# Optimization experiments

Measured on AMD Instinct MI355X. Metric: run time of the kernel, lower is better.

## Reference

```python
import jax, jax.numpy as jnp
import numpy as np

EPS = 1e-12  # F.normalize eps

def _layer(x, adj, y, mask, w, b):
    # support = x @ W
    support = x @ w
    a = adj * mask
    # row-wise L1 normalize: a / max(sum|a|, eps)
    norm = jnp.maximum(jnp.sum(jnp.abs(a), axis=1, keepdims=True), EPS)
    a = a / norm
    out = a @ support + b
    y_hat = a @ y
    return out, y_hat

def setup_inputs() -> dict:
    key = jax.random.key(0)
    ks = jax.random.split(key, 9)
    N, F, H, C = 8192, 512, 256, 40
    stdv1 = 1.0 / np.sqrt(H)
    stdv2 = 1.0 / np.sqrt(C)
    return {
        "x": jax.random.normal(ks[0], (N, F), jnp.float32),
        "adj": jax.random.uniform(ks[1], (N, N), jnp.float32),
        "y": jax.random.uniform(ks[2], (N, C), jnp.float32),
        "mask1": jax.random.uniform(ks[3], (N, N), jnp.float32),
        "mask2": jax.random.uniform(ks[4], (N, N), jnp.float32),
        "w1": jax.random.uniform(ks[5], (F, H), jnp.float32, -stdv1, stdv1),
        "b1": jax.random.uniform(ks[6], (H,), jnp.float32, -stdv1, stdv1),
        "w2": jax.random.uniform(ks[7], (H, C), jnp.float32, -stdv2, stdv2),
        "b2": jax.random.uniform(ks[8], (C,), jnp.float32, -stdv2, stdv2),
    }

def reference(x, adj, y, mask1, mask2, w1, b1, w2, b2):
    h, y_hat = _layer(x, adj, y, mask1, w1, b1)
    h = jax.nn.relu(h)  # dropout is identity in eval mode
    h, y_hat = _layer(h, adj, y_hat, mask2, w2, b2)
    return jax.nn.log_softmax(h, axis=1), jax.nn.log_softmax(y_hat, axis=1)
```

## Files before the change

kernel.cpp:

```cpp
#include <hip/hip_runtime.h>
#include <cstdint>
#include <cstddef>

typedef float f32x4 __attribute__((ext_vector_type(4)));
typedef __bf16 bf16x8_t __attribute__((ext_vector_type(8)));
typedef short s16x8_t __attribute__((ext_vector_type(8)));
typedef unsigned short u16x4_t __attribute__((ext_vector_type(4)));

#define NN 8192
#define FD 512
#define HD 256
#define CD 40

static __device__ __forceinline__ unsigned short f2bf(float f) {
    unsigned int u = __builtin_bit_cast(unsigned int, f);
    u += 0x7FFFu + ((u >> 16) & 1u);
    return (unsigned short)(u >> 16);
}
static __device__ __forceinline__ float bf2f(unsigned short s) {
    unsigned int u = ((unsigned int)s) << 16;
    return __builtin_bit_cast(float, u);
}

typedef __attribute__((address_space(3))) unsigned int lds_u32_t;
typedef __attribute__((address_space(1))) const unsigned int gbl_u32_t;
static __device__ __forceinline__ void gload16(const void* g, const void* lds) {
    __builtin_amdgcn_global_load_lds((gbl_u32_t*)g, (lds_u32_t*)lds, 16, 0, 0);
}

__global__ __launch_bounds__(256) void k_prep_xw1(
        const float* __restrict__ adj,
        const float* __restrict__ mask1,
        const float* __restrict__ mask2,
        unsigned short* __restrict__ P1,
        unsigned short* __restrict__ P2,
        float* __restrict__ sinv1,
        float* __restrict__ sinv2,
        const float* __restrict__ x,
        const float* __restrict__ w1,
        float* __restrict__ sup1) {
    __shared__ float xs[64][36];
    __shared__ float ws[32][68];
    __shared__ float red1[4], red2[4];
    const int t = threadIdx.x;

    if (blockIdx.x < 512) {
        const int bid = blockIdx.x;
        const int m0 = (bid >> 2) * 64;
        const int n0 = (bid & 3) * 64;
        const int tx = t & 15, ty = t >> 4;
        float acc[4][4] = {};
        for (int k0 = 0; k0 < FD; k0 += 32) {
            for (int i = t; i < 512; i += 256) {
                int r = i >> 3, c = (i & 7) << 2;
                *(float4*)&xs[r][c] = *(const float4*)&x[(size_t)(m0 + r) * FD + k0 + c];
            }
            for (int i = t; i < 512; i += 256) {
                int r = i >> 4, c = (i & 15) << 2;
                *(float4*)&ws[r][c] = *(const float4*)&w1[(size_t)(k0 + r) * HD + n0 + c];
            }
            __syncthreads();
            for (int k = 0; k < 32; ++k) {
                float a_[4], b_[4];
                #pragma unroll
                for (int i = 0; i < 4; ++i) a_[i] = xs[ty * 4 + i][k];
                #pragma unroll
                for (int j = 0; j < 4; ++j) b_[j] = ws[k][tx * 4 + j];
                #pragma unroll
                for (int i = 0; i < 4; ++i)
                    #pragma unroll
                    for (int j = 0; j < 4; ++j) acc[i][j] += a_[i] * b_[j];
            }
            __syncthreads();
        }
        #pragma unroll
        for (int i = 0; i < 4; ++i)
            #pragma unroll
            for (int j = 0; j < 4; ++j)
                sup1[(size_t)(m0 + ty * 4 + i) * HD + n0 + tx * 4 + j] = acc[i][j];
        return;
    }

    const int row = blockIdx.x - 512;
    const f32x4* __restrict__ ar  = (const f32x4*)(adj   + (size_t)row * NN);
    const f32x4* __restrict__ m1r = (const f32x4*)(mask1 + (size_t)row * NN);
    const f32x4* __restrict__ m2r = mask2 ? (const f32x4*)(mask2 + (size_t)row * NN) : nullptr;
    float s1 = 0.f, s2 = 0.f;

    f32x4 a  = __builtin_nontemporal_load(&ar[t]);
    f32x4 m1 = __builtin_nontemporal_load(&m1r[t]);
    f32x4 m2 = {};
    if (m2r) m2 = __builtin_nontemporal_load(&m2r[t]);

    #pragma unroll
    for (int j = 0; j < 8; ++j) {
        const int idx = j * 256 + t;
        f32x4 an = {}, m1n = {}, m2n = {};
        if (j < 7) {
            an  = __builtin_nontemporal_load(&ar[idx + 256]);
            m1n = __builtin_nontemporal_load(&m1r[idx + 256]);
            if (m2r) m2n = __builtin_nontemporal_load(&m2r[idx + 256]);
        }
        {
            const float p0 = a[0] * m1[0], p1 = a[1] * m1[1], p2 = a[2] * m1[2], p3 = a[3] * m1[3];
            s1 += fabsf(p0) + fabsf(p1) + fabsf(p2) + fabsf(p3);
            u16x4_t pk; pk.x = f2bf(p0); pk.y = f2bf(p1); pk.z = f2bf(p2); pk.w = f2bf(p3);
            *(u16x4_t*)&P1[(size_t)row * NN + idx * 4] = pk;
        }
        if (m2r) {
            const float p0 = a[0] * m2[0], p1 = a[1] * m2[1], p2 = a[2] * m2[2], p3 = a[3] * m2[3];
            s2 += fabsf(p0) + fabsf(p1) + fabsf(p2) + fabsf(p3);
            u16x4_t pk; pk.x = f2bf(p0); pk.y = f2bf(p1); pk.z = f2bf(p2); pk.w = f2bf(p3);
            *(u16x4_t*)&P2[(size_t)row * NN + idx * 4] = pk;
        }
        a = an; m1 = m1n; m2 = m2n;
    }
    #pragma unroll
    for (int d = 32; d; d >>= 1) { s1 += __shfl_xor(s1, d, 64); s2 += __shfl_xor(s2, d, 64); }
    if ((t & 63) == 0) { red1[t >> 6] = s1; red2[t >> 6] = s2; }
    __syncthreads();
    if (t == 0) {
        const float a1 = red1[0] + red1[1] + red1[2] + red1[3];
        sinv1[row] = 1.0f / fmaxf(a1, 1e-12f);
        if (sinv2) {
            const float a2 = red2[0] + red2[1] + red2[2] + red2[3];
            sinv2[row] = 1.0f / fmaxf(a2, 1e-12f);
        }
    }
}

__global__ __launch_bounds__(256) void k_prep(const float* __restrict__ adj,
                                              const float* __restrict__ mask1,
                                              const float* __restrict__ mask2,
                                              unsigned short* __restrict__ P1,
                                              unsigned short* __restrict__ P2,
                                              float* __restrict__ sinv1,
                                              float* __restrict__ sinv2) {
    const int row = blockIdx.x;
    const int t = threadIdx.x;
    const f32x4* __restrict__ ar  = (const f32x4*)(adj   + (size_t)row * NN);
    const f32x4* __restrict__ m1r = (const f32x4*)(mask1 + (size_t)row * NN);
    const f32x4* __restrict__ m2r = mask2 ? (const f32x4*)(mask2 + (size_t)row * NN) : nullptr;
    float s1 = 0.f, s2 = 0.f;

    f32x4 a  = __builtin_nontemporal_load(&ar[t]);
    f32x4 m1 = __builtin_nontemporal_load(&m1r[t]);
    f32x4 m2 = {};
    if (m2r) m2 = __builtin_nontemporal_load(&m2r[t]);

    #pragma unroll
    for (int j = 0; j < 8; ++j) {
        const int idx = j * 256 + t;
        f32x4 an = {}, m1n = {}, m2n = {};
        if (j < 7) {
            an  = __builtin_nontemporal_load(&ar[idx + 256]);
            m1n = __builtin_nontemporal_load(&m1r[idx + 256]);
            if (m2r) m2n = __builtin_nontemporal_load(&m2r[idx + 256]);
        }
        {
            const float p0 = a[0] * m1[0], p1 = a[1] * m1[1], p2 = a[2] * m1[2], p3 = a[3] * m1[3];
            s1 += fabsf(p0) + fabsf(p1) + fabsf(p2) + fabsf(p3);
            u16x4_t pk; pk.x = f2bf(p0); pk.y = f2bf(p1); pk.z = f2bf(p2); pk.w = f2bf(p3);
            *(u16x4_t*)&P1[(size_t)row * NN + idx * 4] = pk;
        }
        if (m2r) {
            const float p0 = a[0] * m2[0], p1 = a[1] * m2[1], p2 = a[2] * m2[2], p3 = a[3] * m2[3];
            s2 += fabsf(p0) + fabsf(p1) + fabsf(p2) + fabsf(p3);
            u16x4_t pk; pk.x = f2bf(p0); pk.y = f2bf(p1); pk.z = f2bf(p2); pk.w = f2bf(p3);
            *(u16x4_t*)&P2[(size_t)row * NN + idx * 4] = pk;
        }
        a = an; m1 = m1n; m2 = m2n;
    }
    __shared__ float red1[4], red2[4];
    #pragma unroll
    for (int d = 32; d; d >>= 1) { s1 += __shfl_xor(s1, d, 64); s2 += __shfl_xor(s2, d, 64); }
    if ((t & 63) == 0) { red1[t >> 6] = s1; red2[t >> 6] = s2; }
    __syncthreads();
    if (t == 0) {
        const float a1 = red1[0] + red1[1] + red1[2] + red1[3];
        sinv1[row] = 1.0f / fmaxf(a1, 1e-12f);
        if (sinv2) {
            const float a2 = red2[0] + red2[1] + red2[2] + red2[3];
            sinv2[row] = 1.0f / fmaxf(a2, 1e-12f);
        }
    }
}

__global__ __launch_bounds__(256) void k_packB1T(const float* __restrict__ sup1,
                                                 const float* __restrict__ y,
                                                 unsigned short* __restrict__ B1T) {
    __shared__ float tl[64][33];
    const int kt = blockIdx.x & 127;
    const int nt = blockIdx.x >> 7;
    const int k0 = kt * 64, n0 = nt * 32;
    const int t = threadIdx.x;
    {
        const int kr = t >> 2, cb = (t & 3) * 8;
        #pragma unroll
        for (int j = 0; j < 8; ++j) {
            const int n = n0 + cb + j;
            float v;
            if (n < 256)      v = sup1[(size_t)(k0 + kr) * HD + n];
            else if (n < 296) v = y[(size_t)(k0 + kr) * CD + (n - 256)];
            else              v = 0.f;
            tl[kr][cb + j] = v;
        }
    }
    __syncthreads();
    {
        const int nr = t >> 3, part = t & 7;
        unsigned short tmp[8];
        #pragma unroll
        for (int j = 0; j < 8; ++j) tmp[j] = f2bf(tl[part * 8 + j][nr]);
        *(s16x8_t*)&B1T[(size_t)(n0 + nr) * NN + k0 + part * 8] = *(s16x8_t*)tmp;
    }
}

template<int BN, int WM, int WN, int SPLIT, int NTILES>
__global__ __launch_bounds__(256) void k_gemm(const unsigned short* __restrict__ A,
                                              const unsigned short* __restrict__ Bt,
                                              float* __restrict__ Cp) {
    constexpr int BM = 128, BK = 64;
    constexpr int MF = BM / (WM * 16);
    constexpr int NF = BN / (WN * 16);
    constexpr int NBI = BN / 32;
    constexpr int NSTR = NTILES * BN;
    constexpr int MT = NN / BM;
    __shared__ unsigned short As[BM * BK];
    __shared__ unsigned short Bs[BN * BK];
    int mt, ks, nt;
    if constexpr (NTILES > 1) {
        constexpr int NXCD = 8;
        constexpr int PAIRS = MT * SPLIT;
        static_assert(PAIRS % NXCD == 0, "pair count must split across XCDs");
        constexpr int PPX = PAIRS / NXCD;
        const int L = blockIdx.x;
        const int x = L % NXCD, q = L / NXCD;
        const int pr = x * PPX + q / NTILES;
        nt = q % NTILES;
        mt = pr / SPLIT;
        ks = pr % SPLIT;
    } else {
        int b = blockIdx.x;
        nt = 0;
        ks = b % SPLIT;  b /= SPLIT;
        mt = b;
    }
    const int m0 = mt * BM, n0 = nt * BN;
    const int t = threadIdx.x, w = t >> 6, ln = t & 63;
    const int wn = w % WN, wm = w / WN;
    const int lrow = ln & 15, lkq = ln >> 4;
    const int kbeg = ks * (NN / SPLIT), kend = kbeg + (NN / SPLIT);

    f32x4 acc[MF][NF] = {};
    for (int kb = kbeg; kb < kend; kb += BK) {
        #pragma unroll
        for (int i = 0; i < 4; ++i) {
            const int off = (w * 4 + i) * 1024 + ln * 16;
            const int r = off >> 7, ch = (off >> 4) & 7;
            gload16(A + (size_t)(m0 + r) * NN + kb + ((ch ^ (r & 7)) << 3),
                    &As[(w * 4 + i) * 512]);
        }
        #pragma unroll
        for (int i = 0; i < NBI; ++i) {
            const int off = (w * NBI + i) * 1024 + ln * 16;
            const int r = off >> 7, ch = (off >> 4) & 7;
            gload16(Bt + (size_t)(n0 + r) * NN + kb + ((ch ^ (r & 7)) << 3),
                    &Bs[(w * NBI + i) * 512]);
        }
        __syncthreads();

        bf16x8_t af[MF][2];
        #pragma unroll
        for (int mf = 0; mf < MF; ++mf)
            #pragma unroll
            for (int kh = 0; kh < 2; ++kh) {
                const int r = wm * (MF * 16) + mf * 16 + lrow;
                const int ch = (kh * 4 + lkq) ^ (r & 7);
                af[mf][kh] = __builtin_bit_cast(bf16x8_t, *(const s16x8_t*)&As[r * 64 + ch * 8]);
            }
        bf16x8_t bfr[NF][2];
        #pragma unroll
        for (int nf = 0; nf < NF; ++nf)
            #pragma unroll
            for (int kh = 0; kh < 2; ++kh) {
                const int r = wn * (NF * 16) + nf * 16 + lrow;
                const int ch = (kh * 4 + lkq) ^ (r & 7);
                bfr[nf][kh] = __builtin_bit_cast(bf16x8_t, *(const s16x8_t*)&Bs[r * 64 + ch * 8]);
            }
        #pragma unroll
        for (int kh = 0; kh < 2; ++kh)
            #pragma unroll
            for (int mf = 0; mf < MF; ++mf)
                #pragma unroll
                for (int nf = 0; nf < NF; ++nf)
                    acc[mf][nf] = __builtin_amdgcn_mfma_f32_16x16x32_bf16(
                        af[mf][kh], bfr[nf][kh], acc[mf][nf], 0, 0, 0);
        __syncthreads();
    }
    #pragma unroll
    for (int mf = 0; mf < MF; ++mf)
        #pragma unroll
        for (int nf = 0; nf < NF; ++nf)
            #pragma unroll
            for (int e = 0; e < 4; ++e) {
                const int m = m0 + wm * (MF * 16) + mf * 16 + lkq * 4 + e;
                const int n = n0 + wn * (NF * 16) + nf * 16 + lrow;
                Cp[((size_t)ks * NN + m) * NSTR + n] = acc[mf][nf][e];
            }
}

__global__ __launch_bounds__(256) void k_finC(const float* __restrict__ U,
                                              const float* __restrict__ sinv1,
                                              const float* __restrict__ b1,
                                              unsigned short* __restrict__ h1,
                                              unsigned short* __restrict__ B2T) {
    const int t = threadIdx.x;
    const int r = t >> 3, l8 = t & 7;
    const int m = blockIdx.x * 32 + r;
    const float si = sinv1[m];
    const float* __restrict__ u0 = U + (size_t)m * 320;
    const float* __restrict__ u1 = U + (size_t)(NN + m) * 320;
    #pragma unroll
    for (int i = 0; i < 10; ++i) {
        const int c = (l8 + i * 8) * 4;
        f32x4 a = *(const f32x4*)&u0[c];
        f32x4 b = *(const f32x4*)&u1[c];
        f32x4 v;
        #pragma unroll
        for (int e = 0; e < 4; ++e) v[e] = (a[e] + b[e]) * si;
        if (i < 8) {
            u16x4_t pk;
            #pragma unroll
            for (int e = 0; e < 4; ++e) {
                const float hv = fmaxf(v[e] + b1[c + e], 0.f);
                ((unsigned short*)&pk)[e] = f2bf(hv);
            }
            *(u16x4_t*)&h1[(size_t)m * HD + c] = pk;
        } else {
            #pragma unroll
            for (int e = 0; e < 4; ++e) {
                const int cc = c + e;
                if (cc < 296) B2T[(size_t)(40 + cc - 256) * NN + m] = f2bf(v[e]);
            }
        }
    }
}

__global__ __launch_bounds__(256) void k_hw2(const unsigned short* __restrict__ h1,
                                             const float* __restrict__ w2,
                                             unsigned short* __restrict__ B2T) {
    __shared__ float w2s[HD * CD];
    __shared__ unsigned short h1s[32][264];
    __shared__ float ot[CD][33];
    const int t = threadIdx.x;
    const int mb = blockIdx.x * 32;
    for (int i = t; i < HD * CD; i += 256) w2s[i] = w2[i];
    for (int i = t; i < 1024; i += 256) {
        const int r = i >> 5, c = (i & 31) * 8;
        *(s16x8_t*)&h1s[r][c] = *(const s16x8_t*)&h1[(size_t)(mb + r) * HD + c];
    }
    __syncthreads();
    const int m = t >> 3, n0 = t & 7;
    float a5[5] = {};
    for (int k = 0; k < HD; ++k) {
        const float hv = bf2f(h1s[m][k]);
        #pragma unroll
        for (int j = 0; j < 5; ++j) a5[j] += hv * w2s[k * CD + n0 + 8 * j];
    }
    #pragma unroll
    for (int j = 0; j < 5; ++j) ot[n0 + 8 * j][m] = a5[j];
    __syncthreads();
    for (int i = t; i < CD * 32; i += 256) {
        const int n = i >> 5, mm = i & 31;
        B2T[(size_t)n * NN + mb + mm] = f2bf(ot[n][mm]);
    }
    for (int i = t; i < 16 * 32; i += 256)
        B2T[(size_t)(80 + (i >> 5)) * NN + mb + (i & 31)] = 0;
}

__global__ __launch_bounds__(256) void k_finD(const float* __restrict__ U,
                                              const float* __restrict__ sinv2,
                                              const float* __restrict__ b2,
                                              float* __restrict__ out) {
    __shared__ float vt[32][100];
    const int t = threadIdx.x;
    const int mb = blockIdx.x * 32;
    for (int i = t; i < 32 * 24; i += 256) {
        const int r = i / 24, f4 = i % 24;
        const int m = mb + r;
        f32x4 s = {};
        #pragma unroll
        for (int p = 0; p < 8; ++p) {
            f32x4 v = *(const f32x4*)&U[((size_t)p * NN + m) * 96 + f4 * 4];
            #pragma unroll
            for (int e = 0; e < 4; ++e) s[e] += v[e];
        }
        const float si = sinv2[m];
        #pragma unroll
        for (int e = 0; e < 4; ++e) {
            const int c = f4 * 4 + e;
            float v = s[e] * si;
            if (c < CD) v += b2[c];
            vt[r][c] = v;
        }
    }
    __syncthreads();
    const int l8 = t & 7;
    #pragma unroll
    for (int pass = 0; pass < 2; ++pass) {
        const int task = pass * 32 + (t >> 3);
        const int row = task & 31, mat = task >> 5;
        float vals[5];
        float mx = -3.0e38f;
        #pragma unroll
        for (int j = 0; j < 5; ++j) { vals[j] = vt[row][mat * CD + l8 + 8 * j]; mx = fmaxf(mx, vals[j]); }
        mx = fmaxf(mx, __shfl_xor(mx, 4, 8));
        mx = fmaxf(mx, __shfl_xor(mx, 2, 8));
        mx = fmaxf(mx, __shfl_xor(mx, 1, 8));
        float se = 0.f;
        #pragma unroll
        for (int j = 0; j < 5; ++j) se += expf(vals[j] - mx);
        se += __shfl_xor(se, 4, 8);
        se += __shfl_xor(se, 2, 8);
        se += __shfl_xor(se, 1, 8);
        const float ls = logf(se);
        float* op = out + (size_t)mat * (NN * CD) + (size_t)(mb + row) * CD;
        #pragma unroll
        for (int j = 0; j < 5; ++j) op[l8 + 8 * j] = vals[j] - mx - ls;
    }
}

extern "C" void kernel_launch(void* const* d_in, const int* in_sizes, int n_in,
                              void* d_out, int out_size, void* d_ws, size_t ws_size,
                              hipStream_t stream) {
    (void)in_sizes; (void)n_in; (void)out_size;
    const float* x     = (const float*)d_in[0];
    const float* adj   = (const float*)d_in[1];
    const float* y     = (const float*)d_in[2];
    const float* mask1 = (const float*)d_in[3];
    const float* mask2 = (const float*)d_in[4];
    const float* w1    = (const float*)d_in[5];
    const float* b1    = (const float*)d_in[6];
    const float* w2    = (const float*)d_in[7];
    const float* b2    = (const float*)d_in[8];
    float* out = (float*)d_out;

    const bool both = ws_size >= 313065472ULL;
    char* p = (char*)d_ws;
    unsigned short* P1 = (unsigned short*)p; p += 134217728;
    unsigned short* P2 = P1;
    if (both) { P2 = (unsigned short*)p; p += 134217728; }
    float*          sup1 = (float*)p;          p += 8388608;
    unsigned short* B1T  = (unsigned short*)p; p += 5242880;
    unsigned short* h1   = (unsigned short*)p; p += 4194304;
    unsigned short* B2T  = (unsigned short*)p; p += 1572864;
    float*          U    = (float*)p;          p += 25165824;
    float*          sinv1 = (float*)p;         p += 32768;
    float*          sinv2 = (float*)p;         p += 32768;

    if (both) {
        hipLaunchKernelGGL(k_prep_xw1, dim3(8704), dim3(256), 0, stream,
                           adj, mask1, mask2, P1, P2, sinv1, sinv2, x, w1, sup1);
    } else {
        hipLaunchKernelGGL(k_prep_xw1, dim3(8704), dim3(256), 0, stream,
                           adj, mask1, (const float*)nullptr, P1, (unsigned short*)nullptr,
                           sinv1, (float*)nullptr, x, w1, sup1);
    }
    hipLaunchKernelGGL(k_packB1T, dim3(1280), dim3(256), 0, stream, sup1, y, B1T);
    hipLaunchKernelGGL(HIP_KERNEL_NAME(k_gemm<64, 2, 2, 2, 5>), dim3(640), dim3(256), 0, stream,
                       P1, B1T, U);
    hipLaunchKernelGGL(k_finC,    dim3(256),  dim3(256), 0, stream, U, sinv1, b1, h1, B2T);
    hipLaunchKernelGGL(k_hw2,     dim3(256),  dim3(256), 0, stream, h1, w2, B2T);
    if (!both) {
        hipLaunchKernelGGL(k_prep, dim3(8192), dim3(256), 0, stream,
                           adj, mask2, (const float*)nullptr, P1, (unsigned short*)nullptr,
                           sinv2, (float*)nullptr);
    }
    hipLaunchKernelGGL(HIP_KERNEL_NAME(k_gemm<96, 4, 1, 8, 1>), dim3(512), dim3(256), 0, stream,
                       P2, B2T, U);
    hipLaunchKernelGGL(k_finD,    dim3(256),  dim3(256), 0, stream, U, sinv2, b2, out);
}
```

Baseline: 357.3 us.

## Fuse B1T packing into prep kernel and merge finC with hw2

The x@W1 tiles in the prep kernel now transpose through shared memory and write bf16 directly into B1T. Extra blocks in the same launch pack y into B1T and zero its padding rows, so the sup1 buffer and the separate pack kernel go away. finC and hw2 are merged so h1 stays in shared memory instead of round-tripping through global memory. This removes two launches and several intermediate global writes and reads, at the cost of more shared-memory reuse and a larger heterogeneous grid.

```diff
diff --git a/kernel.cpp b/kernel.cpp
--- a/kernel.cpp
+++ b/kernel.cpp
@@ -38,13 +38,14 @@
         float* __restrict__ sinv2,
         const float* __restrict__ x,
         const float* __restrict__ w1,
-        float* __restrict__ sup1) {
-    __shared__ float xs[64][36];
-    __shared__ float ws[32][68];
-    __shared__ float red1[4], red2[4];
+        const float* __restrict__ y,
+        unsigned short* __restrict__ B1T) {
+    __shared__ char smem[18432];
     const int t = threadIdx.x;
 
     if (blockIdx.x < 512) {
+        float (*xs)[36] = (float(*)[36])smem;
+        float (*ws)[68] = (float(*)[68])(smem + 9216);
         const int bid = blockIdx.x;
         const int m0 = (bid >> 2) * 64;
         const int n0 = (bid & 3) * 64;
@@ -73,15 +74,51 @@
             }
             __syncthreads();
         }
+        float (*ot)[65] = (float(*)[65])smem;
         #pragma unroll
         for (int i = 0; i < 4; ++i)
             #pragma unroll
             for (int j = 0; j < 4; ++j)
-                sup1[(size_t)(m0 + ty * 4 + i) * HD + n0 + tx * 4 + j] = acc[i][j];
+                ot[tx * 4 + j][ty * 4 + i] = acc[i][j];
+        __syncthreads();
+        #pragma unroll
+        for (int u = 0; u < 2; ++u) {
+            const int task = t + u * 256;
+            const int nr = task >> 3, part = task & 7;
+            unsigned short tmp[8];
+            #pragma unroll
+            for (int j = 0; j < 8; ++j) tmp[j] = f2bf(ot[nr][part * 8 + j]);
+            *(s16x8_t*)&B1T[(size_t)(n0 + nr) * NN + m0 + part * 8] = *(s16x8_t*)tmp;
+        }
         return;
     }
 
-    const int row = blockIdx.x - 512;
+    if (blockIdx.x < 640) {
+        float (*tl)[41] = (float(*)[41])smem;
+        const int k0 = (blockIdx.x - 512) * 64;
+        for (int u = 0; u < 10; ++u) {
+            const int idx = t + u * 256;
+            tl[idx / 40][idx % 40] = y[(size_t)k0 * CD + idx];
+        }
+        __syncthreads();
+        for (int task = t; task < 320; task += 256) {
+            const int c = task >> 3, part = task & 7;
+            unsigned short tmp[8];
+            #pragma unroll
+            for (int j = 0; j < 8; ++j) tmp[j] = f2bf(tl[part * 8 + j][c]);
+            *(s16x8_t*)&B1T[(size_t)(256 + c) * NN + k0 + part * 8] = *(s16x8_t*)tmp;
+        }
+        for (int task = t; task < 192; task += 256) {
+            const int row = 296 + (task >> 3), part = task & 7;
+            s16x8_t z = {};
+            *(s16x8_t*)&B1T[(size_t)row * NN + k0 + part * 8] = z;
+        }
+        return;
+    }
+
+    float* red1 = (float*)smem;
+    float* red2 = (float*)(smem + 16);
+    const int row = blockIdx.x - 640;
     const f32x4* __restrict__ ar  = (const f32x4*)(adj   + (size_t)row * NN);
     const f32x4* __restrict__ m1r = (const f32x4*)(mask1 + (size_t)row * NN);
     const f32x4* __restrict__ m2r = mask2 ? (const f32x4*)(mask2 + (size_t)row * NN) : nullptr;
@@ -183,36 +220,6 @@
             const float a2 = red2[0] + red2[1] + red2[2] + red2[3];
             sinv2[row] = 1.0f / fmaxf(a2, 1e-12f);
         }
-    }
-}
-
-__global__ __launch_bounds__(256) void k_packB1T(const float* __restrict__ sup1,
-                                                 const float* __restrict__ y,
-                                                 unsigned short* __restrict__ B1T) {
-    __shared__ float tl[64][33];
-    const int kt = blockIdx.x & 127;
-    const int nt = blockIdx.x >> 7;
-    const int k0 = kt * 64, n0 = nt * 32;
-    const int t = threadIdx.x;
-    {
-        const int kr = t >> 2, cb = (t & 3) * 8;
-        #pragma unroll
-        for (int j = 0; j < 8; ++j) {
-            const int n = n0 + cb + j;
-            float v;
-            if (n < 256)      v = sup1[(size_t)(k0 + kr) * HD + n];
-            else if (n < 296) v = y[(size_t)(k0 + kr) * CD + (n - 256)];
-            else              v = 0.f;
-            tl[kr][cb + j] = v;
-        }
-    }
-    __syncthreads();
-    {
-        const int nr = t >> 3, part = t & 7;
-        unsigned short tmp[8];
-        #pragma unroll
-        for (int j = 0; j < 8; ++j) tmp[j] = f2bf(tl[part * 8 + j][nr]);
-        *(s16x8_t*)&B1T[(size_t)(n0 + nr) * NN + k0 + part * 8] = *(s16x8_t*)tmp;
     }
 }
 
@@ -310,70 +317,67 @@
             }
 }
 
-__global__ __launch_bounds__(256) void k_finC(const float* __restrict__ U,
-                                              const float* __restrict__ sinv1,
-                                              const float* __restrict__ b1,
-                                              unsigned short* __restrict__ h1,
-                                              unsigned short* __restrict__ B2T) {
-    const int t = threadIdx.x;
-    const int r = t >> 3, l8 = t & 7;
-    const int m = blockIdx.x * 32 + r;
-    const float si = sinv1[m];
-    const float* __restrict__ u0 = U + (size_t)m * 320;
-    const float* __restrict__ u1 = U + (size_t)(NN + m) * 320;
-    #pragma unroll
-    for (int i = 0; i < 10; ++i) {
-        const int c = (l8 + i * 8) * 4;
-        f32x4 a = *(const f32x4*)&u0[c];
-        f32x4 b = *(const f32x4*)&u1[c];
-        f32x4 v;
-        #pragma unroll
-        for (int e = 0; e < 4; ++e) v[e] = (a[e] + b[e]) * si;
-        if (i < 8) {
-            u16x4_t pk;
-            #pragma unroll
-            for (int e = 0; e < 4; ++e) {
-                const float hv = fmaxf(v[e] + b1[c + e], 0.f);
-                ((unsigned short*)&pk)[e] = f2bf(hv);
-            }
-            *(u16x4_t*)&h1[(size_t)m * HD + c] = pk;
-        } else {
-            #pragma unroll
-            for (int e = 0; e < 4; ++e) {
-                const int cc = c + e;
-                if (cc < 296) B2T[(size_t)(40 + cc - 256) * NN + m] = f2bf(v[e]);
-            }
-        }
-    }
-}
-
-__global__ __launch_bounds__(256) void k_hw2(const unsigned short* __restrict__ h1,
-                                             const float* __restrict__ w2,
-                                             unsigned short* __restrict__ B2T) {
+__global__ __launch_bounds__(256) void k_finC2(const float* __restrict__ U,
+                                               const float* __restrict__ sinv1,
+                                               const float* __restrict__ b1,
+                                               const float* __restrict__ w2,
+                                               unsigned short* __restrict__ B2T) {
     __shared__ float w2s[HD * CD];
     __shared__ unsigned short h1s[32][264];
-    __shared__ float ot[CD][33];
+    __shared__ float otp[CD][33];
     const int t = threadIdx.x;
     const int mb = blockIdx.x * 32;
+
     for (int i = t; i < HD * CD; i += 256) w2s[i] = w2[i];
-    for (int i = t; i < 1024; i += 256) {
-        const int r = i >> 5, c = (i & 31) * 8;
-        *(s16x8_t*)&h1s[r][c] = *(const s16x8_t*)&h1[(size_t)(mb + r) * HD + c];
+
+    {
+        const int r = t >> 3, l8 = t & 7;
+        const int m = mb + r;
+        const float si = sinv1[m];
+        const float* __restrict__ u0 = U + (size_t)m * 320;
+        const float* __restrict__ u1 = U + (size_t)(NN + m) * 320;
+        #pragma unroll
+        for (int i = 0; i < 10; ++i) {
+            const int c = (l8 + i * 8) * 4;
+            f32x4 a = *(const f32x4*)&u0[c];
+            f32x4 b = *(const f32x4*)&u1[c];
+            f32x4 v;
+            #pragma unroll
+            for (int e = 0; e < 4; ++e) v[e] = (a[e] + b[e]) * si;
+            if (i < 8) {
+                u16x4_t pk;
+                #pragma unroll
+                for (int e = 0; e < 4; ++e) {
+                    const float hv = fmaxf(v[e] + b1[c + e], 0.f);
+                    ((unsigned short*)&pk)[e] = f2bf(hv);
+                }
+                *(u16x4_t*)&h1s[r][c] = pk;
+            } else {
+                #pragma unroll
+                for (int e = 0; e < 4; ++e) {
+                    const int cc = c + e;
+                    if (cc < 296) B2T[(size_t)(40 + cc - 256) * NN + m] = f2bf(v[e]);
+                }
+            }
+        }
     }
     __syncthreads();
-    const int m = t >> 3, n0 = t & 7;
-    float a5[5] = {};
-    for (int k = 0; k < HD; ++k) {
-        const float hv = bf2f(h1s[m][k]);
-        #pragma unroll
-        for (int j = 0; j < 5; ++j) a5[j] += hv * w2s[k * CD + n0 + 8 * j];
-    }
-    #pragma unroll
-    for (int j = 0; j < 5; ++j) ot[n0 + 8 * j][m] = a5[j];
+
+    {
+        const int m = t >> 3, n0 = t & 7;
+        float a5[5] = {};
+        for (int k = 0; k < HD; ++k) {
+            const float hv = bf2f(h1s[m][k]);
+            #pragma unroll
+            for (int j = 0; j < 5; ++j) a5[j] += hv * w2s[k * CD + n0 + 8 * j];
+        }
+        #pragma unroll
+        for (int j = 0; j < 5; ++j) otp[n0 + 8 * j][m] = a5[j];
+    }
     __syncthreads();
     for (int i = t; i < CD * 32; i += 256) {
         const int n = i >> 5, mm = i & 31;
-        B2T[(size_t)n * NN + mb + mm] = f2bf(ot[n][mm]);
+        B2T[(size_t)n * NN + mb + mm] = f2bf(otp[n][mm]);
     }
     for (int i = t; i < 16 * 32; i += 256)
         B2T[(size_t)(80 + (i >> 5)) * NN + mb + (i & 31)] = 0;
@@ -451,27 +455,23 @@
     unsigned short* P1 = (unsigned short*)p; p += 134217728;
     unsigned short* P2 = P1;
     if (both) { P2 = (unsigned short*)p; p += 134217728; }
-    float*          sup1 = (float*)p;          p += 8388608;
     unsigned short* B1T  = (unsigned short*)p; p += 5242880;
-    unsigned short* h1   = (unsigned short*)p; p += 4194304;
     unsigned short* B2T  = (unsigned short*)p; p += 1572864;
     float*          U    = (float*)p;          p += 25165824;
     float*          sinv1 = (float*)p;         p += 32768;
     float*          sinv2 = (float*)p;         p += 32768;
 
     if (both) {
-        hipLaunchKernelGGL(k_prep_xw1, dim3(8704), dim3(256), 0, stream,
-                           adj, mask1, mask2, P1, P2, sinv1, sinv2, x, w1, sup1);
+        hipLaunchKernelGGL(k_prep_xw1, dim3(8832), dim3(256), 0, stream,
+                           adj, mask1, mask2, P1, P2, sinv1, sinv2, x, w1, y, B1T);
     } else {
-        hipLaunchKernelGGL(k_prep_xw1, dim3(8704), dim3(256), 0, stream,
+        hipLaunchKernelGGL(k_prep_xw1, dim3(8832), dim3(256), 0, stream,
                            adj, mask1, (const float*)nullptr, P1, (unsigned short*)nullptr,
-                           sinv1, (float*)nullptr, x, w1, sup1);
-    }
-    hipLaunchKernelGGL(k_packB1T, dim3(1280), dim3(256), 0, stream, sup1, y, B1T);
+                           sinv1, (float*)nullptr, x, w1, y, B1T);
+    }
     hipLaunchKernelGGL(HIP_KERNEL_NAME(k_gemm<64, 2, 2, 2, 5>), dim3(640), dim3(256), 0, stream,
                        P1, B1T, U);
-    hipLaunchKernelGGL(k_finC,    dim3(256),  dim3(256), 0, stream, U, sinv1, b1, h1, B2T);
-    hipLaunchKernelGGL(k_hw2,     dim3(256),  dim3(256), 0, stream, h1, w2, B2T);
+    hipLaunchKernelGGL(k_finC2,   dim3(256),  dim3(256), 0, stream, U, sinv1, b1, w2, B2T);
     if (!both) {
         hipLaunchKernelGGL(k_prep, dim3(8192), dim3(256), 0, stream,
                            adj, mask2, (const float*)nullptr, P1, (unsigned short*)nullptr,
```

New measurement: 340.3 us. -4.8%, faster.
